# Performance work log

Measured on AMD Instinct MI355X. Metric: run time of the kernel, lower is better.

The kernel has to match this reference:

```python
import jax, jax.numpy as jnp
import numpy as np

B, T, I, H = 512, 512, 256, 250
W_SCALE = 0.06  # ~ xavier_uniform std for these fan-ins, keeps tanh unsaturated


def setup_inputs() -> dict:
    key = jax.random.key(0)
    k1, k2, k3 = jax.random.split(key, 3)
    x = jax.random.normal(k1, (B, T, I), dtype=jnp.float32)
    h = jnp.zeros((B, H), dtype=jnp.float32)
    Wx = jax.random.normal(k2, (H, I), dtype=jnp.float32) * W_SCALE
    Wh = jax.random.normal(k3, (H, H), dtype=jnp.float32) * W_SCALE
    bh = jnp.zeros((H,), dtype=jnp.float32)
    return {"x": x, "h": h, "Wx": Wx, "Wh": Wh, "bh": bh}


def reference(x, h, Wx, Wh, bh):
    # x: [B, T, I] (batch_first=True), h: [B, H]
    # one_step: h' = tanh(x_t @ Wx^T + h @ Wh^T + bh)
    # Precompute input projections for all timesteps in one big GEMM.
    xproj = jnp.einsum("bti,hi->tbh", x, Wx)  # [T, B, H]

    def step(h_prev, xp_t):
        h_new = jnp.tanh(xp_t + h_prev @ Wh.T + bh)
        return h_new, h_new

    _, hs = jax.lax.scan(step, h, xproj)  # hs: [T, B, H]
    return jnp.transpose(hs, (1, 0, 2))  # [B, T, H]
```

## Files before the change

### kernel.cpp

```cpp
#include <hip/hip_runtime.h>

#define B_SZ 512
#define T_SZ 512
#define I_SZ 256
#define H_SZ 250

typedef __bf16 bf16x8 __attribute__((ext_vector_type(8)));
typedef __bf16 bf16x4 __attribute__((ext_vector_type(4)));
typedef float  f32x4  __attribute__((ext_vector_type(4)));

__device__ __forceinline__ float fast_tanh(float x) {
    float ax = __builtin_fabsf(x);
    float e  = __expf(-2.0f * ax);
    float r  = (1.0f - e) / (1.0f + e);
    return __builtin_copysignf(r, x);
}

#define BM 128
#define BN 128
#define BK 32
#define LDT 40

__global__ __launch_bounds__(256, 2) void xproj_kernel(
    const float* __restrict__ x,
    const float* __restrict__ Wx,
    const float* __restrict__ bh,
    float* __restrict__ out)
{
    __shared__ __align__(16) __bf16 As[BM * LDT];
    __shared__ __align__(16) __bf16 Bs[BM * LDT];

    const int chunk = gridDim.x >> 3;
    const int swz   = (blockIdx.x & 7) * chunk + (blockIdx.x >> 3);
    const int bm = swz >> 1;
    const int bn = swz & 1;
    const int m0 = bm * BM;
    const int n0 = bn * BN;

    const int tid  = threadIdx.x;
    const int lane = tid & 63;
    const int wave = tid >> 6;
    const int wm   = wave >> 1;
    const int wn   = wave & 1;
    const int l15  = lane & 15;
    const int quad = lane >> 4;

    f32x4 acc[4][4];
#pragma unroll
    for (int i = 0; i < 4; ++i)
#pragma unroll
        for (int j = 0; j < 4; ++j)
            acc[i][j] = (f32x4){0.f, 0.f, 0.f, 0.f};

    for (int kk = 0; kk < I_SZ / BK; ++kk) {
        __syncthreads();
#pragma unroll
        for (int i = 0; i < 4; ++i) {
            int f   = tid + i * 256;
            int row = f >> 3;
            int c4  = f & 7;
            {
                const float4 v = *(const float4*)&x[(size_t)(m0 + row) * I_SZ + kk * BK + c4 * 4];
                bf16x4 b;
                b[0] = (__bf16)v.x; b[1] = (__bf16)v.y; b[2] = (__bf16)v.z; b[3] = (__bf16)v.w;
                *(bf16x4*)&As[row * LDT + c4 * 4] = b;
            }
            {
                int gr = n0 + row;
                bf16x4 b;
                if (gr < H_SZ) {
                    const float4 v = *(const float4*)&Wx[(size_t)gr * I_SZ + kk * BK + c4 * 4];
                    b[0] = (__bf16)v.x; b[1] = (__bf16)v.y; b[2] = (__bf16)v.z; b[3] = (__bf16)v.w;
                } else {
                    b[0] = (__bf16)0.f; b[1] = (__bf16)0.f; b[2] = (__bf16)0.f; b[3] = (__bf16)0.f;
                }
                *(bf16x4*)&Bs[row * LDT + c4 * 4] = b;
            }
        }
        __syncthreads();

        bf16x8 af[4], bfr[4];
#pragma unroll
        for (int tm = 0; tm < 4; ++tm)
            af[tm] = *(const bf16x8*)&As[(wm * 64 + tm * 16 + l15) * LDT + quad * 8];
#pragma unroll
        for (int tn = 0; tn < 4; ++tn)
            bfr[tn] = *(const bf16x8*)&Bs[(wn * 64 + tn * 16 + l15) * LDT + quad * 8];
#pragma unroll
        for (int tm = 0; tm < 4; ++tm)
#pragma unroll
            for (int tn = 0; tn < 4; ++tn)
                acc[tm][tn] = __builtin_amdgcn_mfma_f32_16x16x32_bf16(af[tm], bfr[tn], acc[tm][tn], 0, 0, 0);
    }

#pragma unroll
    for (int tn = 0; tn < 4; ++tn) {
        int gn = n0 + wn * 64 + tn * 16 + l15;
        if (gn >= H_SZ) continue;
        float bias = bh[gn];
#pragma unroll
        for (int tm = 0; tm < 4; ++tm) {
#pragma unroll
            for (int r = 0; r < 4; ++r) {
                int gm = m0 + wm * 64 + tm * 16 + quad * 4 + r;
                out[(size_t)gm * H_SZ + gn] = acc[tm][tn][r] + bias;
            }
        }
    }
}

#define HLD 264

__global__ __launch_bounds__(512, 2) void rnn_kernel(
    const float* __restrict__ h0,
    const float* __restrict__ Wh,
    float* __restrict__ out)
{
    __shared__ __align__(16) __bf16 hbuf[2][3 * HLD];

    const int b0   = blockIdx.x * 2;
    const int tid  = threadIdx.x;
    const int lane = tid & 63;
    const int wave = tid >> 6;
    const int l15  = lane & 15;
    const int quad = lane >> 4;
    const int j0w  = wave * 32;

    for (int i = tid; i < 2 * 3 * HLD; i += 512)
        ((__bf16*)hbuf)[i] = (__bf16)0.f;
    __syncthreads();

    for (int k = tid; k < H_SZ; k += 512) {
        hbuf[0][0 * HLD + k] = (__bf16)h0[(size_t)(b0 + 0) * H_SZ + k];
        hbuf[0][1 * HLD + k] = (__bf16)h0[(size_t)(b0 + 1) * H_SZ + k];
    }

    bf16x8 wf[2][8];
#pragma unroll
    for (int tl = 0; tl < 2; ++tl) {
        const int j = j0w + tl * 16 + l15;
#pragma unroll
        for (int kt = 0; kt < 8; ++kt) {
            const int kb = kt * 32 + quad * 8;
            bf16x8 v;
#pragma unroll
            for (int e = 0; e < 8; ++e) {
                const int k = kb + e;
                v[e] = (j < H_SZ && k < H_SZ) ? (__bf16)Wh[(size_t)j * H_SZ + k] : (__bf16)0.f;
            }
            wf[tl][kt] = v;
        }
    }
    __syncthreads();

    const int arow = (l15 == 0) ? 0 : ((l15 == 4) ? 1 : 2);
    const int aoff = arow * HLD;
    const int qa   = quad & 1;
    const int woff = qa * HLD;

    bool   act[2];
    int    jj[2];
    float* xptr[2];
#pragma unroll
    for (int tl = 0; tl < 2; ++tl) {
        jj[tl]  = j0w + tl * 16 + l15;
        act[tl] = (quad < 2) && (jj[tl] < H_SZ);
        const int jc = (jj[tl] < H_SZ) ? jj[tl] : 0;
        xptr[tl] = out + (size_t)(b0 + qa) * T_SZ * H_SZ + jc;
    }

    float xc[2], x1[2];
#pragma unroll
    for (int tl = 0; tl < 2; ++tl) {
        xc[tl] = act[tl] ? xptr[tl][0]    : 0.f;
        x1[tl] = act[tl] ? xptr[tl][H_SZ] : 0.f;
    }

    for (int t = 0; t < T_SZ; ++t) {
        const int cur = t & 1;
        const int nxt = cur ^ 1;

        float x2[2];
        const bool pf = (t + 2 < T_SZ);
#pragma unroll
        for (int tl = 0; tl < 2; ++tl)
            x2[tl] = (pf && act[tl]) ? xptr[tl][2 * H_SZ] : 0.f;

        bf16x8 af[8];
#pragma unroll
        for (int kt = 0; kt < 8; ++kt)
            af[kt] = *(const bf16x8*)&hbuf[cur][aoff + kt * 32 + quad * 8];

        f32x4 a0a = (f32x4){0.f, 0.f, 0.f, 0.f};
        f32x4 a0b = (f32x4){0.f, 0.f, 0.f, 0.f};
        f32x4 a1a = (f32x4){0.f, 0.f, 0.f, 0.f};
        f32x4 a1b = (f32x4){0.f, 0.f, 0.f, 0.f};
#pragma unroll
        for (int kt = 0; kt < 4; ++kt) {
            a0a = __builtin_amdgcn_mfma_f32_16x16x32_bf16(af[kt],     wf[0][kt],     a0a, 0, 0, 0);
            a1a = __builtin_amdgcn_mfma_f32_16x16x32_bf16(af[kt],     wf[1][kt],     a1a, 0, 0, 0);
            a0b = __builtin_amdgcn_mfma_f32_16x16x32_bf16(af[kt + 4], wf[0][kt + 4], a0b, 0, 0, 0);
            a1b = __builtin_amdgcn_mfma_f32_16x16x32_bf16(af[kt + 4], wf[1][kt + 4], a1b, 0, 0, 0);
        }

        const float s[2] = { a0a[0] + a0b[0], a1a[0] + a1b[0] };
#pragma unroll
        for (int tl = 0; tl < 2; ++tl) {
            if (act[tl]) {
                float v = fast_tanh(s[tl] + xc[tl]);
                xptr[tl][0] = v;
                hbuf[nxt][woff + jj[tl]] = (__bf16)v;
            }
            xptr[tl] += H_SZ;
            xc[tl] = x1[tl];
            x1[tl] = x2[tl];
        }

        asm volatile("s_waitcnt lgkmcnt(0)" ::: "memory");
        __builtin_amdgcn_s_barrier();
        asm volatile("" ::: "memory");
    }
}

extern "C" void kernel_launch(void* const* d_in, const int* in_sizes, int n_in,
                              void* d_out, int out_size, void* d_ws, size_t ws_size,
                              hipStream_t stream) {
    const float* x  = (const float*)d_in[0];
    const float* h  = (const float*)d_in[1];
    const float* Wx = (const float*)d_in[2];
    const float* Wh = (const float*)d_in[3];
    const float* bh = (const float*)d_in[4];
    float* out = (float*)d_out;

    const int M = B_SZ * T_SZ;
    xproj_kernel<<<dim3((M / BM) * 2), dim3(256), 0, stream>>>(x, Wx, bh, out);
    rnn_kernel<<<dim3(B_SZ / 2), dim3(512), 0, stream>>>(h, Wh, out);
}
```

Measured before the change: 930.3 us.

## Widen xproj tile to full H and run one batch row per RNN block

The input-projection GEMM now uses a 128x256 tile that covers all of H, so each x tile is loaded and converted once instead of twice, and the grid swizzle is dropped. The recurrent kernel changes from 2 batch rows per 512-thread block to 1 batch row per 256-thread block, launching 512 blocks. Each wave now owns 64 output columns and holds 4 weight fragments in registers. The h buffer uses a new interleaved layout, so lane 0 reads the real row and the other lanes read a zero row. This spreads the serial recurrence over more CUs with smaller barriers, at the cost of more register pressure and twice as many blocks each loading the whole Wh matrix.

```diff
diff --git a/kernel.cpp b/kernel.cpp
--- a/kernel.cpp
+++ b/kernel.cpp
@@ -17,7 +17,7 @@
 }
 
 #define BM 128
-#define BN 128
+#define BN 256
 #define BK 32
 #define LDT 40
 
@@ -28,14 +28,9 @@
     float* __restrict__ out)
 {
     __shared__ __align__(16) __bf16 As[BM * LDT];
-    __shared__ __align__(16) __bf16 Bs[BM * LDT];
-
-    const int chunk = gridDim.x >> 3;
-    const int swz   = (blockIdx.x & 7) * chunk + (blockIdx.x >> 3);
-    const int bm = swz >> 1;
-    const int bn = swz & 1;
-    const int m0 = bm * BM;
-    const int n0 = bn * BN;
+    __shared__ __align__(16) __bf16 Bs[BN * LDT];
+
+    const int m0 = blockIdx.x * BM;
 
     const int tid  = threadIdx.x;
     const int lane = tid & 63;
@@ -45,11 +40,11 @@
     const int l15  = lane & 15;
     const int quad = lane >> 4;
 
-    f32x4 acc[4][4];
+    f32x4 acc[4][8];
 #pragma unroll
     for (int i = 0; i < 4; ++i)
 #pragma unroll
-        for (int j = 0; j < 4; ++j)
+        for (int j = 0; j < 8; ++j)
             acc[i][j] = (f32x4){0.f, 0.f, 0.f, 0.f};
 
     for (int kk = 0; kk < I_SZ / BK; ++kk) {
@@ -59,43 +54,44 @@
             int f   = tid + i * 256;
             int row = f >> 3;
             int c4  = f & 7;
-            {
-                const float4 v = *(const float4*)&x[(size_t)(m0 + row) * I_SZ + kk * BK + c4 * 4];
-                bf16x4 b;
+            const float4 v = *(const float4*)&x[(size_t)(m0 + row) * I_SZ + kk * BK + c4 * 4];
+            bf16x4 b;
+            b[0] = (__bf16)v.x; b[1] = (__bf16)v.y; b[2] = (__bf16)v.z; b[3] = (__bf16)v.w;
+            *(bf16x4*)&As[row * LDT + c4 * 4] = b;
+        }
+#pragma unroll
+        for (int i = 0; i < 8; ++i) {
+            int f   = tid + i * 256;
+            int row = f >> 3;
+            int c4  = f & 7;
+            bf16x4 b;
+            if (row < H_SZ) {
+                const float4 v = *(const float4*)&Wx[(size_t)row * I_SZ + kk * BK + c4 * 4];
                 b[0] = (__bf16)v.x; b[1] = (__bf16)v.y; b[2] = (__bf16)v.z; b[3] = (__bf16)v.w;
-                *(bf16x4*)&As[row * LDT + c4 * 4] = b;
-            }
-            {
-                int gr = n0 + row;
-                bf16x4 b;
-                if (gr < H_SZ) {
-                    const float4 v = *(const float4*)&Wx[(size_t)gr * I_SZ + kk * BK + c4 * 4];
-                    b[0] = (__bf16)v.x; b[1] = (__bf16)v.y; b[2] = (__bf16)v.z; b[3] = (__bf16)v.w;
-                } else {
-                    b[0] = (__bf16)0.f; b[1] = (__bf16)0.f; b[2] = (__bf16)0.f; b[3] = (__bf16)0.f;
-                }
-                *(bf16x4*)&Bs[row * LDT + c4 * 4] = b;
-            }
+            } else {
+                b[0] = (__bf16)0.f; b[1] = (__bf16)0.f; b[2] = (__bf16)0.f; b[3] = (__bf16)0.f;
+            }
+            *(bf16x4*)&Bs[row * LDT + c4 * 4] = b;
         }
         __syncthreads();
 
-        bf16x8 af[4], bfr[4];
+        bf16x8 af[4], bfr[8];
 #pragma unroll
         for (int tm = 0; tm < 4; ++tm)
             af[tm] = *(const bf16x8*)&As[(wm * 64 + tm * 16 + l15) * LDT + quad * 8];
 #pragma unroll
-        for (int tn = 0; tn < 4; ++tn)
-            bfr[tn] = *(const bf16x8*)&Bs[(wn * 64 + tn * 16 + l15) * LDT + quad * 8];
+        for (int tn = 0; tn < 8; ++tn)
+            bfr[tn] = *(const bf16x8*)&Bs[(wn * 128 + tn * 16 + l15) * LDT + quad * 8];
 #pragma unroll
         for (int tm = 0; tm < 4; ++tm)
 #pragma unroll
-            for (int tn = 0; tn < 4; ++tn)
+            for (int tn = 0; tn < 8; ++tn)
                 acc[tm][tn] = __builtin_amdgcn_mfma_f32_16x16x32_bf16(af[tm], bfr[tn], acc[tm][tn], 0, 0, 0);
     }
 
 #pragma unroll
-    for (int tn = 0; tn < 4; ++tn) {
-        int gn = n0 + wn * 64 + tn * 16 + l15;
+    for (int tn = 0; tn < 8; ++tn) {
+        int gn = wn * 128 + tn * 16 + l15;
         if (gn >= H_SZ) continue;
         float bias = bh[gn];
 #pragma unroll
@@ -109,35 +105,33 @@
     }
 }
 
-#define HLD 264
-
-__global__ __launch_bounds__(512, 2) void rnn_kernel(
+__global__ __launch_bounds__(256, 2) void rnn_kernel(
     const float* __restrict__ h0,
     const float* __restrict__ Wh,
     float* __restrict__ out)
 {
-    __shared__ __align__(16) __bf16 hbuf[2][3 * HLD];
-
-    const int b0   = blockIdx.x * 2;
+    __shared__ __align__(16) __bf16 hbuf[2][512];
+
+    const int b    = blockIdx.x;
     const int tid  = threadIdx.x;
     const int lane = tid & 63;
     const int wave = tid >> 6;
     const int l15  = lane & 15;
     const int quad = lane >> 4;
-    const int j0w  = wave * 32;
-
-    for (int i = tid; i < 2 * 3 * HLD; i += 512)
+    const int j0w  = wave * 64;
+
+    for (int i = tid; i < 2 * 512; i += 256)
         ((__bf16*)hbuf)[i] = (__bf16)0.f;
     __syncthreads();
 
-    for (int k = tid; k < H_SZ; k += 512) {
-        hbuf[0][0 * HLD + k] = (__bf16)h0[(size_t)(b0 + 0) * H_SZ + k];
-        hbuf[0][1 * HLD + k] = (__bf16)h0[(size_t)(b0 + 1) * H_SZ + k];
-    }
-
-    bf16x8 wf[2][8];
-#pragma unroll
-    for (int tl = 0; tl < 2; ++tl) {
+    for (int k = tid; k < H_SZ; k += 256) {
+        int e = ((k >> 5) << 6) + (((k >> 3) & 3) << 3) + (k & 7);
+        hbuf[0][e] = (__bf16)h0[(size_t)b * H_SZ + k];
+    }
+
+    bf16x8 wf[4][8];
+#pragma unroll
+    for (int tl = 0; tl < 4; ++tl) {
         const int j = j0w + tl * 16 + l15;
 #pragma unroll
         for (int kt = 0; kt < 8; ++kt) {
@@ -153,25 +147,24 @@
     }
     __syncthreads();
 
-    const int arow = (l15 == 0) ? 0 : ((l15 == 4) ? 1 : 2);
-    const int aoff = arow * HLD;
-    const int qa   = quad & 1;
-    const int woff = qa * HLD;
-
-    bool   act[2];
-    int    jj[2];
-    float* xptr[2];
-#pragma unroll
-    for (int tl = 0; tl < 2; ++tl) {
+    const int aoff = (l15 == 0) ? 0 : 32;
+
+    bool   act[4];
+    int    jj[4];
+    int    we[4];
+    float* xptr[4];
+#pragma unroll
+    for (int tl = 0; tl < 4; ++tl) {
         jj[tl]  = j0w + tl * 16 + l15;
-        act[tl] = (quad < 2) && (jj[tl] < H_SZ);
+        act[tl] = (quad == 0) && (jj[tl] < H_SZ);
         const int jc = (jj[tl] < H_SZ) ? jj[tl] : 0;
-        xptr[tl] = out + (size_t)(b0 + qa) * T_SZ * H_SZ + jc;
-    }
-
-    float xc[2], x1[2];
-#pragma unroll
-    for (int tl = 0; tl < 2; ++tl) {
+        we[tl]  = ((jc >> 5) << 6) + (((jc >> 3) & 3) << 3) + (jc & 7);
+        xptr[tl] = out + (size_t)b * T_SZ * H_SZ + jc;
+    }
+
+    float xc[4], x1[4];
+#pragma unroll
+    for (int tl = 0; tl < 4; ++tl) {
         xc[tl] = act[tl] ? xptr[tl][0]    : 0.f;
         x1[tl] = act[tl] ? xptr[tl][H_SZ] : 0.f;
     }
@@ -180,36 +173,39 @@
         const int cur = t & 1;
         const int nxt = cur ^ 1;
 
-        float x2[2];
+        float x2[4];
         const bool pf = (t + 2 < T_SZ);
 #pragma unroll
-        for (int tl = 0; tl < 2; ++tl)
+        for (int tl = 0; tl < 4; ++tl)
             x2[tl] = (pf && act[tl]) ? xptr[tl][2 * H_SZ] : 0.f;
 
         bf16x8 af[8];
 #pragma unroll
         for (int kt = 0; kt < 8; ++kt)
-            af[kt] = *(const bf16x8*)&hbuf[cur][aoff + kt * 32 + quad * 8];
-
-        f32x4 a0a = (f32x4){0.f, 0.f, 0.f, 0.f};
-        f32x4 a0b = (f32x4){0.f, 0.f, 0.f, 0.f};
-        f32x4 a1a = (f32x4){0.f, 0.f, 0.f, 0.f};
-        f32x4 a1b = (f32x4){0.f, 0.f, 0.f, 0.f};
+            af[kt] = *(const bf16x8*)&hbuf[cur][kt * 64 + aoff + quad * 8];
+
+        f32x4 aA[4], aB[4];
+#pragma unroll
+        for (int tl = 0; tl < 4; ++tl) {
+            aA[tl] = (f32x4){0.f, 0.f, 0.f, 0.f};
+            aB[tl] = (f32x4){0.f, 0.f, 0.f, 0.f};
+        }
 #pragma unroll
         for (int kt = 0; kt < 4; ++kt) {
-            a0a = __builtin_amdgcn_mfma_f32_16x16x32_bf16(af[kt],     wf[0][kt],     a0a, 0, 0, 0);
-            a1a = __builtin_amdgcn_mfma_f32_16x16x32_bf16(af[kt],     wf[1][kt],     a1a, 0, 0, 0);
-            a0b = __builtin_amdgcn_mfma_f32_16x16x32_bf16(af[kt + 4], wf[0][kt + 4], a0b, 0, 0, 0);
-            a1b = __builtin_amdgcn_mfma_f32_16x16x32_bf16(af[kt + 4], wf[1][kt + 4], a1b, 0, 0, 0);
-        }
-
-        const float s[2] = { a0a[0] + a0b[0], a1a[0] + a1b[0] };
-#pragma unroll
-        for (int tl = 0; tl < 2; ++tl) {
+#pragma unroll
+            for (int tl = 0; tl < 4; ++tl) {
+                aA[tl] = __builtin_amdgcn_mfma_f32_16x16x32_bf16(af[kt],     wf[tl][kt],     aA[tl], 0, 0, 0);
+                aB[tl] = __builtin_amdgcn_mfma_f32_16x16x32_bf16(af[kt + 4], wf[tl][kt + 4], aB[tl], 0, 0, 0);
+            }
+        }
+
+#pragma unroll
+        for (int tl = 0; tl < 4; ++tl) {
+            const float s = aA[tl][0] + aB[tl][0];
             if (act[tl]) {
-                float v = fast_tanh(s[tl] + xc[tl]);
+                float v = fast_tanh(s + xc[tl]);
                 xptr[tl][0] = v;
-                hbuf[nxt][woff + jj[tl]] = (__bf16)v;
+                hbuf[nxt][we[tl]] = (__bf16)v;
             }
             xptr[tl] += H_SZ;
             xc[tl] = x1[tl];
@@ -233,6 +229,6 @@
     float* out = (float*)d_out;
 
     const int M = B_SZ * T_SZ;
-    xproj_kernel<<<dim3((M / BM) * 2), dim3(256), 0, stream>>>(x, Wx, bh, out);
-    rnn_kernel<<<dim3(B_SZ / 2), dim3(512), 0, stream>>>(h, Wh, out);
-}
+    xproj_kernel<<<dim3(M / BM), dim3(256), 0, stream>>>(x, Wx, bh, out);
+    rnn_kernel<<<dim3(B_SZ), dim3(256), 0, stream>>>(h, Wh, out);
+}
```

New measurement: 1.113 ms. 19.6% more time.

## Restructure xproj GEMM to full-K row tiles and interleave RNN hidden-state layout

Applied to the files above, without the earlier changes.

The input-projection GEMM now gives each block 64 rows with the full K=256 of x staged in LDS, and covers all 256 output columns by streaming Wx in 64-wide K chunks. This removes the 2x redundant reads of x across the two N-tiles and cuts the number of K-loop barriers. The RNN kernel stores the two batch rows of h interleaved in 32-element groups (stride 96), which changes the LDS bank pattern of the per-step fragment reads and writes. The cost is more LDS per GEMM block, which may lower occupancy, and a serialized barrier per Wx chunk reload.

```diff
diff --git a/kernel.cpp b/kernel.cpp
--- a/kernel.cpp
+++ b/kernel.cpp
@@ -16,10 +16,9 @@
     return __builtin_copysignf(r, x);
 }
 
-#define BM 128
-#define BN 128
-#define BK 32
-#define LDT 40
+#define XBM 64
+#define LDA 260
+#define LWS 68
 
 __global__ __launch_bounds__(256, 2) void xproj_kernel(
     const float* __restrict__ x,
@@ -27,96 +26,113 @@
     const float* __restrict__ bh,
     float* __restrict__ out)
 {
-    __shared__ __align__(16) __bf16 As[BM * LDT];
-    __shared__ __align__(16) __bf16 Bs[BM * LDT];
-
-    const int chunk = gridDim.x >> 3;
-    const int swz   = (blockIdx.x & 7) * chunk + (blockIdx.x >> 3);
-    const int bm = swz >> 1;
-    const int bn = swz & 1;
-    const int m0 = bm * BM;
-    const int n0 = bn * BN;
-
+    __shared__ __align__(16) __bf16 As[XBM * LDA];
+    __shared__ __align__(16) __bf16 Ws[256 * LWS];
+
+    const int m0   = blockIdx.x * XBM;
     const int tid  = threadIdx.x;
     const int lane = tid & 63;
     const int wave = tid >> 6;
-    const int wm   = wave >> 1;
-    const int wn   = wave & 1;
     const int l15  = lane & 15;
     const int quad = lane >> 4;
+    const int j0w  = wave * 64;
+
+#pragma unroll
+    for (int i = 0; i < 16; ++i) {
+        int f   = tid + i * 256;
+        int row = f >> 6;
+        int c4  = f & 63;
+        const float4 v = *(const float4*)&x[(size_t)(m0 + row) * I_SZ + c4 * 4];
+        bf16x4 b;
+        b[0] = (__bf16)v.x; b[1] = (__bf16)v.y; b[2] = (__bf16)v.z; b[3] = (__bf16)v.w;
+        *(bf16x4*)&As[row * LDA + c4 * 4] = b;
+    }
+#pragma unroll
+    for (int i = 0; i < 16; ++i) {
+        int f   = tid + i * 256;
+        int row = f >> 4;
+        int c4  = f & 15;
+        bf16x4 b;
+        if (row < H_SZ) {
+            const float4 v = *(const float4*)&Wx[(size_t)row * I_SZ + c4 * 4];
+            b[0] = (__bf16)v.x; b[1] = (__bf16)v.y; b[2] = (__bf16)v.z; b[3] = (__bf16)v.w;
+        } else {
+            b[0] = (__bf16)0.f; b[1] = (__bf16)0.f; b[2] = (__bf16)0.f; b[3] = (__bf16)0.f;
+        }
+        *(bf16x4*)&Ws[row * LWS + c4 * 4] = b;
+    }
+    __syncthreads();
 
     f32x4 acc[4][4];
 #pragma unroll
-    for (int i = 0; i < 4; ++i)
-#pragma unroll
-        for (int j = 0; j < 4; ++j)
-            acc[i][j] = (f32x4){0.f, 0.f, 0.f, 0.f};
-
-    for (int kk = 0; kk < I_SZ / BK; ++kk) {
+    for (int a = 0; a < 4; ++a)
+#pragma unroll
+        for (int bq = 0; bq < 4; ++bq)
+            acc[a][bq] = (f32x4){0.f, 0.f, 0.f, 0.f};
+
+    for (int c = 0; c < 4; ++c) {
+        bf16x8 wf[4][2];
+#pragma unroll
+        for (int tl = 0; tl < 4; ++tl)
+#pragma unroll
+            for (int kt = 0; kt < 2; ++kt)
+                wf[tl][kt] = *(const bf16x8*)&Ws[(j0w + tl * 16 + l15) * LWS + kt * 32 + quad * 8];
         __syncthreads();
-#pragma unroll
-        for (int i = 0; i < 4; ++i) {
-            int f   = tid + i * 256;
-            int row = f >> 3;
-            int c4  = f & 7;
-            {
-                const float4 v = *(const float4*)&x[(size_t)(m0 + row) * I_SZ + kk * BK + c4 * 4];
+
+        if (c < 3) {
+#pragma unroll
+            for (int i = 0; i < 16; ++i) {
+                int f   = tid + i * 256;
+                int row = f >> 4;
+                int c4  = f & 15;
                 bf16x4 b;
-                b[0] = (__bf16)v.x; b[1] = (__bf16)v.y; b[2] = (__bf16)v.z; b[3] = (__bf16)v.w;
-                *(bf16x4*)&As[row * LDT + c4 * 4] = b;
-            }
-            {
-                int gr = n0 + row;
-                bf16x4 b;
-                if (gr < H_SZ) {
-                    const float4 v = *(const float4*)&Wx[(size_t)gr * I_SZ + kk * BK + c4 * 4];
+                if (row < H_SZ) {
+                    const float4 v = *(const float4*)&Wx[(size_t)row * I_SZ + (c + 1) * 64 + c4 * 4];
                     b[0] = (__bf16)v.x; b[1] = (__bf16)v.y; b[2] = (__bf16)v.z; b[3] = (__bf16)v.w;
                 } else {
                     b[0] = (__bf16)0.f; b[1] = (__bf16)0.f; b[2] = (__bf16)0.f; b[3] = (__bf16)0.f;
                 }
-                *(bf16x4*)&Bs[row * LDT + c4 * 4] = b;
-            }
+                *(bf16x4*)&Ws[row * LWS + c4 * 4] = b;
+            }
+        }
+
+#pragma unroll
+        for (int tm = 0; tm < 4; ++tm) {
+            bf16x8 af[2];
+#pragma unroll
+            for (int kt = 0; kt < 2; ++kt)
+                af[kt] = *(const bf16x8*)&As[(tm * 16 + l15) * LDA + c * 64 + kt * 32 + quad * 8];
+#pragma unroll
+            for (int kt = 0; kt < 2; ++kt)
+#pragma unroll
+                for (int tl = 0; tl < 4; ++tl)
+                    acc[tm][tl] = __builtin_amdgcn_mfma_f32_16x16x32_bf16(af[kt], wf[tl][kt], acc[tm][tl], 0, 0, 0);
         }
         __syncthreads();
-
-        bf16x8 af[4], bfr[4];
-#pragma unroll
-        for (int tm = 0; tm < 4; ++tm)
-            af[tm] = *(const bf16x8*)&As[(wm * 64 + tm * 16 + l15) * LDT + quad * 8];
-#pragma unroll
-        for (int tn = 0; tn < 4; ++tn)
-            bfr[tn] = *(const bf16x8*)&Bs[(wn * 64 + tn * 16 + l15) * LDT + quad * 8];
-#pragma unroll
-        for (int tm = 0; tm < 4; ++tm)
-#pragma unroll
-            for (int tn = 0; tn < 4; ++tn)
-                acc[tm][tn] = __builtin_amdgcn_mfma_f32_16x16x32_bf16(af[tm], bfr[tn], acc[tm][tn], 0, 0, 0);
-    }
-
-#pragma unroll
-    for (int tn = 0; tn < 4; ++tn) {
-        int gn = n0 + wn * 64 + tn * 16 + l15;
+    }
+
+#pragma unroll
+    for (int tl = 0; tl < 4; ++tl) {
+        int gn = j0w + tl * 16 + l15;
         if (gn >= H_SZ) continue;
         float bias = bh[gn];
 #pragma unroll
         for (int tm = 0; tm < 4; ++tm) {
 #pragma unroll
             for (int r = 0; r < 4; ++r) {
-                int gm = m0 + wm * 64 + tm * 16 + quad * 4 + r;
-                out[(size_t)gm * H_SZ + gn] = acc[tm][tn][r] + bias;
-            }
-        }
-    }
-}
-
-#define HLD 264
+                int gm = m0 + tm * 16 + quad * 4 + r;
+                out[(size_t)gm * H_SZ + gn] = acc[tm][tl][r] + bias;
+            }
+        }
+    }
+}
 
 __global__ __launch_bounds__(512, 2) void rnn_kernel(
     const float* __restrict__ h0,
     const float* __restrict__ Wh,
     float* __restrict__ out)
 {
-    __shared__ __align__(16) __bf16 hbuf[2][3 * HLD];
+    __shared__ __align__(16) __bf16 hbuf[2][768];
 
     const int b0   = blockIdx.x * 2;
     const int tid  = threadIdx.x;
@@ -126,13 +142,14 @@
     const int quad = lane >> 4;
     const int j0w  = wave * 32;
 
-    for (int i = tid; i < 2 * 3 * HLD; i += 512)
+    for (int i = tid; i < 2 * 768; i += 512)
         ((__bf16*)hbuf)[i] = (__bf16)0.f;
     __syncthreads();
 
     for (int k = tid; k < H_SZ; k += 512) {
-        hbuf[0][0 * HLD + k] = (__bf16)h0[(size_t)(b0 + 0) * H_SZ + k];
-        hbuf[0][1 * HLD + k] = (__bf16)h0[(size_t)(b0 + 1) * H_SZ + k];
+        int e = ((k >> 5) * 96) + (((k >> 3) & 3) << 3) + (k & 7);
+        hbuf[0][e +  0] = (__bf16)h0[(size_t)(b0 + 0) * H_SZ + k];
+        hbuf[0][e + 32] = (__bf16)h0[(size_t)(b0 + 1) * H_SZ + k];
     }
 
     bf16x8 wf[2][8];
@@ -153,19 +170,19 @@
     }
     __syncthreads();
 
-    const int arow = (l15 == 0) ? 0 : ((l15 == 4) ? 1 : 2);
-    const int aoff = arow * HLD;
+    const int aoff = (l15 == 0) ? 0 : ((l15 == 4) ? 32 : 64);
     const int qa   = quad & 1;
-    const int woff = qa * HLD;
 
     bool   act[2];
     int    jj[2];
+    int    we[2];
     float* xptr[2];
 #pragma unroll
     for (int tl = 0; tl < 2; ++tl) {
         jj[tl]  = j0w + tl * 16 + l15;
         act[tl] = (quad < 2) && (jj[tl] < H_SZ);
         const int jc = (jj[tl] < H_SZ) ? jj[tl] : 0;
+        we[tl]  = ((jc >> 5) * 96) + qa * 32 + (((jc >> 3) & 3) << 3) + (jc & 7);
         xptr[tl] = out + (size_t)(b0 + qa) * T_SZ * H_SZ + jc;
     }
 
@@ -189,7 +206,7 @@
         bf16x8 af[8];
 #pragma unroll
         for (int kt = 0; kt < 8; ++kt)
-            af[kt] = *(const bf16x8*)&hbuf[cur][aoff + kt * 32 + quad * 8];
+            af[kt] = *(const bf16x8*)&hbuf[cur][kt * 96 + aoff + quad * 8];
 
         f32x4 a0a = (f32x4){0.f, 0.f, 0.f, 0.f};
         f32x4 a0b = (f32x4){0.f, 0.f, 0.f, 0.f};
@@ -209,7 +226,7 @@
             if (act[tl]) {
                 float v = fast_tanh(s[tl] + xc[tl]);
                 xptr[tl][0] = v;
-                hbuf[nxt][woff + jj[tl]] = (__bf16)v;
+                hbuf[nxt][we[tl]] = (__bf16)v;
             }
             xptr[tl] += H_SZ;
             xc[tl] = x1[tl];
@@ -233,6 +250,6 @@
     float* out = (float*)d_out;
 
     const int M = B_SZ * T_SZ;
-    xproj_kernel<<<dim3((M / BM) * 2), dim3(256), 0, stream>>>(x, Wx, bh, out);
+    xproj_kernel<<<dim3(M / XBM), dim3(256), 0, stream>>>(x, Wx, bh, out);
     rnn_kernel<<<dim3(B_SZ / 2), dim3(512), 0, stream>>>(h, Wh, out);
 }
```

Measured after the change: 933.4 us. No clear change (+0.3%).

## Fuse input projection into recurrent kernel with per-step x MFMA

Applied to the files above, without the earlier changes.

Removes the separate xproj GEMM kernel. Each timestep, the recurrent kernel now stages the next x row into shared memory as bf16 and computes x_t·Wx^T with MFMAs against register-resident Wx fragments, alongside the h·Wh^T product. Shared buffers get an interleaved layout, and the step loop is unrolled by two with fixed buffer indices. This avoids writing and reading back the full projection array, but it adds 16 more MFMAs and an x load to every serial step, and holding both weight sets in registers raises register pressure.

```diff
diff --git a/kernel.cpp b/kernel.cpp
--- a/kernel.cpp
+++ b/kernel.cpp
@@ -6,7 +6,6 @@
 #define H_SZ 250
 
 typedef __bf16 bf16x8 __attribute__((ext_vector_type(8)));
-typedef __bf16 bf16x4 __attribute__((ext_vector_type(4)));
 typedef float  f32x4  __attribute__((ext_vector_type(4)));
 
 __device__ __forceinline__ float fast_tanh(float x) {
@@ -16,107 +15,16 @@
     return __builtin_copysignf(r, x);
 }
 
-#define BM 128
-#define BN 128
-#define BK 32
-#define LDT 40
-
-__global__ __launch_bounds__(256, 2) void xproj_kernel(
+__global__ __launch_bounds__(512, 2) void rnn_fused(
     const float* __restrict__ x,
+    const float* __restrict__ h0,
     const float* __restrict__ Wx,
+    const float* __restrict__ Wh,
     const float* __restrict__ bh,
     float* __restrict__ out)
 {
-    __shared__ __align__(16) __bf16 As[BM * LDT];
-    __shared__ __align__(16) __bf16 Bs[BM * LDT];
-
-    const int chunk = gridDim.x >> 3;
-    const int swz   = (blockIdx.x & 7) * chunk + (blockIdx.x >> 3);
-    const int bm = swz >> 1;
-    const int bn = swz & 1;
-    const int m0 = bm * BM;
-    const int n0 = bn * BN;
-
-    const int tid  = threadIdx.x;
-    const int lane = tid & 63;
-    const int wave = tid >> 6;
-    const int wm   = wave >> 1;
-    const int wn   = wave & 1;
-    const int l15  = lane & 15;
-    const int quad = lane >> 4;
-
-    f32x4 acc[4][4];
-#pragma unroll
-    for (int i = 0; i < 4; ++i)
-#pragma unroll
-        for (int j = 0; j < 4; ++j)
-            acc[i][j] = (f32x4){0.f, 0.f, 0.f, 0.f};
-
-    for (int kk = 0; kk < I_SZ / BK; ++kk) {
-        __syncthreads();
-#pragma unroll
-        for (int i = 0; i < 4; ++i) {
-            int f   = tid + i * 256;
-            int row = f >> 3;
-            int c4  = f & 7;
-            {
-                const float4 v = *(const float4*)&x[(size_t)(m0 + row) * I_SZ + kk * BK + c4 * 4];
-                bf16x4 b;
-                b[0] = (__bf16)v.x; b[1] = (__bf16)v.y; b[2] = (__bf16)v.z; b[3] = (__bf16)v.w;
-                *(bf16x4*)&As[row * LDT + c4 * 4] = b;
-            }
-            {
-                int gr = n0 + row;
-                bf16x4 b;
-                if (gr < H_SZ) {
-                    const float4 v = *(const float4*)&Wx[(size_t)gr * I_SZ + kk * BK + c4 * 4];
-                    b[0] = (__bf16)v.x; b[1] = (__bf16)v.y; b[2] = (__bf16)v.z; b[3] = (__bf16)v.w;
-                } else {
-                    b[0] = (__bf16)0.f; b[1] = (__bf16)0.f; b[2] = (__bf16)0.f; b[3] = (__bf16)0.f;
-                }
-                *(bf16x4*)&Bs[row * LDT + c4 * 4] = b;
-            }
-        }
-        __syncthreads();
-
-        bf16x8 af[4], bfr[4];
-#pragma unroll
-        for (int tm = 0; tm < 4; ++tm)
-            af[tm] = *(const bf16x8*)&As[(wm * 64 + tm * 16 + l15) * LDT + quad * 8];
-#pragma unroll
-        for (int tn = 0; tn < 4; ++tn)
-            bfr[tn] = *(const bf16x8*)&Bs[(wn * 64 + tn * 16 + l15) * LDT + quad * 8];
-#pragma unroll
-        for (int tm = 0; tm < 4; ++tm)
-#pragma unroll
-            for (int tn = 0; tn < 4; ++tn)
-                acc[tm][tn] = __builtin_amdgcn_mfma_f32_16x16x32_bf16(af[tm], bfr[tn], acc[tm][tn], 0, 0, 0);
-    }
-
-#pragma unroll
-    for (int tn = 0; tn < 4; ++tn) {
-        int gn = n0 + wn * 64 + tn * 16 + l15;
-        if (gn >= H_SZ) continue;
-        float bias = bh[gn];
-#pragma unroll
-        for (int tm = 0; tm < 4; ++tm) {
-#pragma unroll
-            for (int r = 0; r < 4; ++r) {
-                int gm = m0 + wm * 64 + tm * 16 + quad * 4 + r;
-                out[(size_t)gm * H_SZ + gn] = acc[tm][tn][r] + bias;
-            }
-        }
-    }
-}
-
-#define HLD 264
-
-__global__ __launch_bounds__(512, 2) void rnn_kernel(
-    const float* __restrict__ h0,
-    const float* __restrict__ Wh,
-    float* __restrict__ out)
-{
-    __shared__ __align__(16) __bf16 hbuf[2][3 * HLD];
+    __shared__ __align__(16) __bf16 hbuf[2][768];
+    __shared__ __align__(16) __bf16 xbuf[2][768];
 
     const int b0   = blockIdx.x * 2;
     const int tid  = threadIdx.x;
@@ -126,99 +34,117 @@
     const int quad = lane >> 4;
     const int j0w  = wave * 32;
 
-    for (int i = tid; i < 2 * 3 * HLD; i += 512)
+    for (int i = tid; i < 2 * 768; i += 512) {
         ((__bf16*)hbuf)[i] = (__bf16)0.f;
-    __syncthreads();
+        ((__bf16*)xbuf)[i] = (__bf16)0.f;
+    }
 
     for (int k = tid; k < H_SZ; k += 512) {
-        hbuf[0][0 * HLD + k] = (__bf16)h0[(size_t)(b0 + 0) * H_SZ + k];
-        hbuf[0][1 * HLD + k] = (__bf16)h0[(size_t)(b0 + 1) * H_SZ + k];
+        int e = ((k >> 5) * 96) + (((k >> 3) & 3) << 3) + (k & 7);
+        hbuf[0][e +  0] = (__bf16)h0[(size_t)(b0 + 0) * H_SZ + k];
+        hbuf[0][e + 32] = (__bf16)h0[(size_t)(b0 + 1) * H_SZ + k];
     }
 
-    bf16x8 wf[2][8];
+    const int xsel = tid >> 8;
+    const int xk   = tid & 255;
+    const int xe   = ((xk >> 5) * 96) + xsel * 32 + (((xk >> 3) & 3) << 3) + (xk & 7);
+    const float* xg = x + (size_t)(b0 + xsel) * T_SZ * I_SZ + xk;
+    xbuf[0][xe] = (__bf16)xg[0];
+    xg += I_SZ;
+
+    bf16x8 wfh[2][8], wfx[2][8];
+    float  bhv[2];
 #pragma unroll
     for (int tl = 0; tl < 2; ++tl) {
-        const int j = j0w + tl * 16 + l15;
+        const int  j  = j0w + tl * 16 + l15;
+        const bool jv = (j < H_SZ);
+        bhv[tl] = jv ? bh[j] : 0.f;
 #pragma unroll
         for (int kt = 0; kt < 8; ++kt) {
             const int kb = kt * 32 + quad * 8;
-            bf16x8 v;
+            bf16x8 vh, vx;
 #pragma unroll
             for (int e = 0; e < 8; ++e) {
                 const int k = kb + e;
-                v[e] = (j < H_SZ && k < H_SZ) ? (__bf16)Wh[(size_t)j * H_SZ + k] : (__bf16)0.f;
+                vh[e] = (jv && k < H_SZ) ? (__bf16)Wh[(size_t)j * H_SZ + k] : (__bf16)0.f;
+                vx[e] = jv               ? (__bf16)Wx[(size_t)j * I_SZ + k] : (__bf16)0.f;
             }
-            wf[tl][kt] = v;
+            wfh[tl][kt] = vh;
+            wfx[tl][kt] = vx;
         }
     }
     __syncthreads();
 
-    const int arow = (l15 == 0) ? 0 : ((l15 == 4) ? 1 : 2);
-    const int aoff = arow * HLD;
+    const int aoff = (l15 == 0) ? 0 : ((l15 == 4) ? 32 : 64);
     const int qa   = quad & 1;
-    const int woff = qa * HLD;
 
     bool   act[2];
-    int    jj[2];
-    float* xptr[2];
+    int    we[2];
+    float* outp[2];
 #pragma unroll
     for (int tl = 0; tl < 2; ++tl) {
-        jj[tl]  = j0w + tl * 16 + l15;
-        act[tl] = (quad < 2) && (jj[tl] < H_SZ);
-        const int jc = (jj[tl] < H_SZ) ? jj[tl] : 0;
-        xptr[tl] = out + (size_t)(b0 + qa) * T_SZ * H_SZ + jc;
+        const int j = j0w + tl * 16 + l15;
+        act[tl] = (quad < 2) && (j < H_SZ);
+        const int jc = (j < H_SZ) ? j : 0;
+        we[tl]  = ((jc >> 5) * 96) + qa * 32 + (((jc >> 3) & 3) << 3) + (jc & 7);
+        outp[tl] = out + (size_t)(b0 + qa) * T_SZ * H_SZ + jc;
     }
 
-    float xc[2], x1[2];
+    const f32x4 vzero = (f32x4){0.f, 0.f, 0.f, 0.f};
+
+    auto step = [&](int t, int cur, int nxt) {
+        const bool pf = (t + 1 < T_SZ);
+        float xv = 0.f;
+        if (pf) xv = xg[0];
+
+        bf16x8 axf[8];
 #pragma unroll
-    for (int tl = 0; tl < 2; ++tl) {
-        xc[tl] = act[tl] ? xptr[tl][0]    : 0.f;
-        x1[tl] = act[tl] ? xptr[tl][H_SZ] : 0.f;
-    }
-
-    for (int t = 0; t < T_SZ; ++t) {
-        const int cur = t & 1;
-        const int nxt = cur ^ 1;
-
-        float x2[2];
-        const bool pf = (t + 2 < T_SZ);
+        for (int kt = 0; kt < 8; ++kt)
+            axf[kt] = *(const bf16x8*)&xbuf[cur][kt * 96 + aoff + quad * 8];
+        f32x4 cx[2], ch[2];
 #pragma unroll
         for (int tl = 0; tl < 2; ++tl)
-            x2[tl] = (pf && act[tl]) ? xptr[tl][2 * H_SZ] : 0.f;
+            cx[tl] = __builtin_amdgcn_mfma_f32_16x16x32_bf16(axf[0], wfx[tl][0], vzero, 0, 0, 0);
+#pragma unroll
+        for (int kt = 1; kt < 8; ++kt)
+#pragma unroll
+            for (int tl = 0; tl < 2; ++tl)
+                cx[tl] = __builtin_amdgcn_mfma_f32_16x16x32_bf16(axf[kt], wfx[tl][kt], cx[tl], 0, 0, 0);
 
-        bf16x8 af[8];
+        bf16x8 ahf[8];
 #pragma unroll
         for (int kt = 0; kt < 8; ++kt)
-            af[kt] = *(const bf16x8*)&hbuf[cur][aoff + kt * 32 + quad * 8];
+            ahf[kt] = *(const bf16x8*)&hbuf[cur][kt * 96 + aoff + quad * 8];
+#pragma unroll
+        for (int tl = 0; tl < 2; ++tl)
+            ch[tl] = __builtin_amdgcn_mfma_f32_16x16x32_bf16(ahf[0], wfh[tl][0], vzero, 0, 0, 0);
+#pragma unroll
+        for (int kt = 1; kt < 8; ++kt)
+#pragma unroll
+            for (int tl = 0; tl < 2; ++tl)
+                ch[tl] = __builtin_amdgcn_mfma_f32_16x16x32_bf16(ahf[kt], wfh[tl][kt], ch[tl], 0, 0, 0);
 
-        f32x4 a0a = (f32x4){0.f, 0.f, 0.f, 0.f};
-        f32x4 a0b = (f32x4){0.f, 0.f, 0.f, 0.f};
-        f32x4 a1a = (f32x4){0.f, 0.f, 0.f, 0.f};
-        f32x4 a1b = (f32x4){0.f, 0.f, 0.f, 0.f};
 #pragma unroll
-        for (int kt = 0; kt < 4; ++kt) {
-            a0a = __builtin_amdgcn_mfma_f32_16x16x32_bf16(af[kt],     wf[0][kt],     a0a, 0, 0, 0);
-            a1a = __builtin_amdgcn_mfma_f32_16x16x32_bf16(af[kt],     wf[1][kt],     a1a, 0, 0, 0);
-            a0b = __builtin_amdgcn_mfma_f32_16x16x32_bf16(af[kt + 4], wf[0][kt + 4], a0b, 0, 0, 0);
-            a1b = __builtin_amdgcn_mfma_f32_16x16x32_bf16(af[kt + 4], wf[1][kt + 4], a1b, 0, 0, 0);
+        for (int tl = 0; tl < 2; ++tl) {
+            const float v = fast_tanh(cx[tl][0] + ch[tl][0] + bhv[tl]);
+            if (act[tl]) {
+                hbuf[nxt][we[tl]] = (__bf16)v;
+                outp[tl][0] = v;
+            }
+            outp[tl] += H_SZ;
         }
 
-        const float s[2] = { a0a[0] + a0b[0], a1a[0] + a1b[0] };
-#pragma unroll
-        for (int tl = 0; tl < 2; ++tl) {
-            if (act[tl]) {
-                float v = fast_tanh(s[tl] + xc[tl]);
-                xptr[tl][0] = v;
-                hbuf[nxt][woff + jj[tl]] = (__bf16)v;
-            }
-            xptr[tl] += H_SZ;
-            xc[tl] = x1[tl];
-            x1[tl] = x2[tl];
-        }
+        if (pf) xbuf[nxt][xe] = (__bf16)xv;
+        xg += I_SZ;
 
         asm volatile("s_waitcnt lgkmcnt(0)" ::: "memory");
         __builtin_amdgcn_s_barrier();
         asm volatile("" ::: "memory");
+    };
+
+    for (int t = 0; t < T_SZ; t += 2) {
+        step(t,     0, 1);
+        step(t + 1, 1, 0);
     }
 }
 
@@ -232,7 +158,5 @@
     const float* bh = (const float*)d_in[4];
     float* out = (float*)d_out;
 
-    const int M = B_SZ * T_SZ;
-    xproj_kernel<<<dim3((M / BM) * 2), dim3(256), 0, stream>>>(x, Wx, bh, out);
-    rnn_kernel<<<dim3(B_SZ / 2), dim3(512), 0, stream>>>(h, Wh, out);
+    rnn_fused<<<dim3(B_SZ / 2), dim3(512), 0, stream>>>(x, h, Wx, Wh, bh, out);
 }
```

Measured after the change: 1.005 ms. +8.0%, slower.
